# Performance work log

Hardware: AMD Instinct MI355X
Metric: run time of the kernel (lower is better)

The kernel has to match this reference:

```python
import jax, jax.numpy as jnp
import numpy as np

L, D, H, G = 3, 64, 4, 64            # layers, hidden_dim, heads, num_graphs
N, E = 20000, 320000                  # nodes, edges
HD = H * D                            # heads * out_channels = 256
DENSE = 256
EPS = 1e-5


def setup_inputs() -> dict:
    key = jax.random.key(0)
    ks = jax.random.split(key, 32)
    s = 0.05
    f32 = jnp.float32
    inp = {
        "x": jax.random.normal(ks[0], (N, D), f32),
        "edge_attr": jax.random.normal(ks[1], (E, D), f32),
        "edge_index": jax.random.randint(ks[2], (2, E), 0, N, dtype=jnp.int32),
        "batch": ((jnp.arange(N, dtype=jnp.int32) * G) // N).astype(jnp.int32),
        # per-layer TransformerConv params (stacked over layer dim)
        "Wq": jax.random.normal(ks[3], (L, D, HD), f32) * s,
        "bq": jnp.zeros((L, HD), f32),
        "Wk": jax.random.normal(ks[4], (L, D, HD), f32) * s,
        "bk": jnp.zeros((L, HD), f32),
        "Wv": jax.random.normal(ks[5], (L, D, HD), f32) * s,
        "bv": jnp.zeros((L, HD), f32),
        "We": jax.random.normal(ks[6], (L, D, HD), f32) * s,   # lin_edge (no bias in PyG)
        "Wskip": jax.random.normal(ks[7], (L, D, HD), f32) * s,
        "bskip": jnp.zeros((L, HD), f32),
        "bn_gamma": jnp.ones((L, HD), f32),
        "bn_beta": jnp.zeros((L, HD), f32),
        "Wt": jax.random.normal(ks[8], (L, HD, D), f32) * s,   # transf_layers
        "bt": jnp.zeros((L, D), f32),
        # MLP head
        "W1": jax.random.normal(ks[9], (2 * D, DENSE), f32) * s,
        "b1": jnp.zeros((DENSE,), f32),
        "W2": jax.random.normal(ks[10], (DENSE, DENSE // 2), f32) * s,
        "b2": jnp.zeros((DENSE // 2,), f32),
        "W3": jax.random.normal(ks[11], (DENSE // 2, 1), f32) * s,
        "b3": jnp.zeros((1,), f32),
    }
    return inp


def _transformer_conv(x, edge_attr, src, dst, Wq, bq, Wk, bk, Wv, bv, We, Wskip, bskip):
    # PyG TransformerConv, concat=True, beta=False, root_weight=True, eval (no attn dropout)
    q = (x @ Wq + bq).reshape(N, H, D)[dst]                 # [E,H,C]
    k = (x @ Wk + bk).reshape(N, H, D)[src]                 # [E,H,C]
    v = (x @ Wv + bv).reshape(N, H, D)[src]                 # [E,H,C]
    e = (edge_attr @ We).reshape(E, H, D)                   # [E,H,C]
    k = k + e
    logits = (q * k).sum(-1) / jnp.sqrt(jnp.asarray(D, x.dtype))  # [E,H]
    m = jax.ops.segment_max(logits, dst, num_segments=N)    # stable softmax per dst node
    p = jnp.exp(logits - m[dst])
    z = jax.ops.segment_sum(p, dst, num_segments=N)
    w = p / z[dst]                                          # [E,H]
    msg = w[..., None] * (v + e)                            # [E,H,C]
    agg = jax.ops.segment_sum(msg, dst, num_segments=N).reshape(N, HD)
    return agg + x @ Wskip + bskip                          # [N, H*C]


def _batchnorm(h, gamma, beta):
    mu = h.mean(0)
    var = h.var(0)  # biased, as torch BN uses for normalization
    return (h - mu) * jax.lax.rsqrt(var + EPS) * gamma + beta


def reference(x, edge_attr, edge_index, batch, Wq, bq, Wk, bk, Wv, bv, We, Wskip,
              bskip, bn_gamma, bn_beta, Wt, bt, W1, b1, W2, b2, W3, b3):
    src, dst = edge_index[0], edge_index[1]
    counts = jax.ops.segment_sum(jnp.ones((N,), x.dtype), batch, num_segments=G)
    rep = jnp.zeros((G, 2 * D), x.dtype)
    for i in range(L):
        h = _transformer_conv(x, edge_attr, src, dst, Wq[i], bq[i], Wk[i], bk[i],
                              Wv[i], bv[i], We[i], Wskip[i], bskip[i])
        h = _batchnorm(h, bn_gamma[i], bn_beta[i])
        x = jax.nn.relu(h @ Wt[i] + bt[i])                  # [N, D]
        gmx = jax.ops.segment_max(x, batch, num_segments=G)
        gav = jax.ops.segment_sum(x, batch, num_segments=G) / counts[:, None]
        rep = rep + jnp.concatenate([gmx, gav], axis=1)     # sum of per-layer reps
    out = jax.nn.relu(rep @ W1 + b1)
    out = jax.nn.relu(out @ W2 + b2)
    return out @ W3 + b3                                    # [G, 1]
```

## Files before the change

kernel.cpp:

```cpp
#include <hip/hip_runtime.h>
#include <math.h>
#include <float.h>

#define N_NODES 20000
#define N_PAD 20032
#define N_EDGES 320000
#define NGRAPH 64
#define NLAYER 3
#define BN_EPS 1e-5f

typedef short bf16x8 __attribute__((ext_vector_type(8)));
typedef float f32x4 __attribute__((ext_vector_type(4)));
typedef unsigned short u16x8 __attribute__((ext_vector_type(8)));

__device__ inline unsigned short f2bf(float f) {
    unsigned int u = __float_as_uint(f);
    unsigned int r = u + 0x7FFF + ((u >> 16) & 1);
    return (unsigned short)(r >> 16);
}
__device__ inline float bf2f(unsigned short s) {
    return __uint_as_float((unsigned int)s << 16);
}

__global__ void count_kernel(const int* __restrict__ ei, int* __restrict__ cnt) {
    int e = blockIdx.x * blockDim.x + threadIdx.x;
    if (e < N_EDGES) atomicAdd(&cnt[ei[N_EDGES + e]], 1);
}

__global__ void scan_kernel(const int* __restrict__ cnt, int* __restrict__ rowptr) {
    __shared__ int sh[256];
    int t = threadIdx.x;
    const int CH = (N_NODES + 255) / 256;
    int base = t * CH;
    int s = 0;
    for (int i = 0; i < CH; i++) { int idx = base + i; if (idx < N_NODES) s += cnt[idx]; }
    sh[t] = s;
    __syncthreads();
    for (int off = 1; off < 256; off <<= 1) {
        int v = sh[t];
        int add = (t >= off) ? sh[t - off] : 0;
        __syncthreads();
        sh[t] = v + add;
        __syncthreads();
    }
    int run = sh[t] - s;
    for (int i = 0; i < CH; i++) {
        int idx = base + i;
        if (idx < N_NODES) { rowptr[idx] = run; run += cnt[idx]; }
    }
    if (t == 255) rowptr[N_NODES] = sh[255];
}

__global__ void fill_kernel(const int* __restrict__ ei, const int* __restrict__ rowptr,
                            int* __restrict__ cur, int* __restrict__ eidx,
                            int* __restrict__ esrc) {
    int e = blockIdx.x * blockDim.x + threadIdx.x;
    if (e < N_EDGES) {
        int dst = ei[N_EDGES + e];
        int pos = atomicAdd(&cur[dst], 1);
        int slot = rowptr[dst] + pos;
        eidx[slot] = e;
        esrc[slot] = ei[e];
    }
}

__global__ void permute_ea_b_kernel(const float* __restrict__ edge_attr,
                                    const int* __restrict__ eidx,
                                    unsigned short* __restrict__ eaPb) {
    int idx = blockIdx.x * blockDim.x + threadIdx.x;
    if (idx < N_EDGES * 16) {
        int j = idx >> 4, c4 = idx & 15;
        float4 v = *(const float4*)(edge_attr + (size_t)eidx[j] * 64 + c4 * 4);
        ((ushort4*)eaPb)[idx] = make_ushort4(f2bf(v.x), f2bf(v.y), f2bf(v.z), f2bf(v.w));
    }
}

__global__ void wu_kernel(const float* __restrict__ Wq, const float* __restrict__ bq,
                          const float* __restrict__ We,
                          float* __restrict__ Wu, float* __restrict__ bu) {
    int j = blockIdx.x, layer = blockIdx.y;
    int t = threadIdx.x, h = t >> 6, d = t & 63;
    const float* Wql = Wq + layer * 16384;
    const float* Wel = We + layer * 16384;
    float acc = 0.f;
    for (int c = 0; c < 64; c++)
        acc += Wql[j * 256 + h * 64 + c] * Wel[d * 256 + h * 64 + c];
    Wu[layer * 16384 + j * 256 + h * 64 + d] = acc;
    if (j == 0) {
        const float* bql = bq + layer * 256;
        float ab = 0.f;
        for (int c = 0; c < 64; c++) ab += bql[h * 64 + c] * Wel[d * 256 + h * 64 + c];
        bu[layer * 256 + h * 64 + d] = ab;
    }
}

__global__ void wallt_kernel(const float* __restrict__ Wq, const float* __restrict__ Wk,
                             const float* __restrict__ Wv, const float* __restrict__ Ws,
                             const float* __restrict__ Wu,
                             const float* __restrict__ bq, const float* __restrict__ bk,
                             const float* __restrict__ bv, const float* __restrict__ bs,
                             const float* __restrict__ bu,
                             unsigned short* __restrict__ WallT, float* __restrict__ ball) {
    int c = blockIdx.x, l = blockIdx.y, k = threadIdx.x;
    int seg = c >> 8, ci = c & 255;
    const float* W; const float* b;
    switch (seg) {
        case 0:  W = Wq; b = bq; break;
        case 1:  W = Wk; b = bk; break;
        case 2:  W = Wv; b = bv; break;
        case 3:  W = Ws; b = bs; break;
        default: W = Wu; b = bu; break;
    }
    WallT[(size_t)l * 81920 + c * 64 + k] = f2bf(W[l * 16384 + k * 256 + ci]);
    if (k == 0) ball[l * 1280 + c] = b[l * 256 + ci];
}

__global__ void xtobf_kernel(const float* __restrict__ x, unsigned short* __restrict__ xbf) {
    int i4 = blockIdx.x * 256 + threadIdx.x;
    if (i4 >= N_PAD * 64 / 4) return;
    int n = i4 >> 4;
    ushort4 o;
    if (n < N_NODES) {
        float4 v = ((const float4*)x)[i4];
        o = make_ushort4(f2bf(v.x), f2bf(v.y), f2bf(v.z), f2bf(v.w));
    } else o = make_ushort4(0, 0, 0, 0);
    ((ushort4*)xbf)[i4] = o;
}

__global__ __launch_bounds__(256) void gemm_qkvsu2_kernel(
    const unsigned short* __restrict__ xbf,
    const unsigned short* __restrict__ WallT,
    const float* __restrict__ ball,
    unsigned short* __restrict__ qbf, unsigned short* __restrict__ kvbf,
    unsigned short* __restrict__ sbf, unsigned short* __restrict__ ubf) {
    int t = threadIdx.x, wid = t >> 6, lane = t & 63;
    int lrow = lane & 15, lk = lane >> 4;
    int y = blockIdx.y;
    int col0 = y * 64;
    int q = y & 3;
    unsigned short* outp; int ostr, mul, obase;
    if (y < 4)       { outp = qbf;  ostr = 256; mul = 1; obase = q * 64; }
    else if (y < 8)  { outp = kvbf; ostr = 512; mul = 2; obase = q * 128; }
    else if (y < 12) { outp = kvbf; ostr = 512; mul = 2; obase = q * 128 + 1; }
    else if (y < 16) { outp = sbf;  ostr = 256; mul = 1; obase = q * 64; }
    else             { outp = ubf;  ostr = 256; mul = 1; obase = q * 64; }

    bf16x8 bfrag[4][2];
#pragma unroll
    for (int ct = 0; ct < 4; ct++)
#pragma unroll
        for (int kc = 0; kc < 2; kc++)
            bfrag[ct][kc] = *(const bf16x8*)(WallT +
                (size_t)(col0 + ct * 16 + lrow) * 64 + kc * 32 + lk * 8);
    float bias[4];
#pragma unroll
    for (int ct = 0; ct < 4; ct++) bias[ct] = ball[col0 + ct * 16 + lrow];

    for (int nc = blockIdx.x; nc < N_PAD / 64; nc += gridDim.x) {
        int n0 = nc * 64 + wid * 16;
        bf16x8 a0 = *(const bf16x8*)(xbf + (size_t)(n0 + lrow) * 64 + lk * 8);
        bf16x8 a1 = *(const bf16x8*)(xbf + (size_t)(n0 + lrow) * 64 + 32 + lk * 8);
#pragma unroll
        for (int ct = 0; ct < 4; ct++) {
            f32x4 acc = {bias[ct], bias[ct], bias[ct], bias[ct]};
            acc = __builtin_amdgcn_mfma_f32_16x16x32_bf16(a0, bfrag[ct][0], acc, 0, 0, 0);
            acc = __builtin_amdgcn_mfma_f32_16x16x32_bf16(a1, bfrag[ct][1], acc, 0, 0, 0);
            int cl = ct * 16 + lrow;
#pragma unroll
            for (int r = 0; r < 4; r++) {
                int n = n0 + lk * 4 + r;
                if (n < N_NODES)
                    outp[(size_t)n * ostr + obase + cl * mul] = f2bf(acc[r]);
            }
        }
    }
}

__global__ __launch_bounds__(256) void attn6_kernel(
    const unsigned short* __restrict__ eaPb,
    const float* __restrict__ ea_f32,
    const int* __restrict__ eaidx,
    const int* __restrict__ rowptr, const int* __restrict__ esrc,
    const unsigned short* __restrict__ qbf, const unsigned short* __restrict__ ubf,
    const unsigned short* __restrict__ kvbf,
    const unsigned short* __restrict__ sbf,
    unsigned short* __restrict__ hskb,
    unsigned short* __restrict__ raccb) {
    int t = threadIdx.x;
    int wid = t >> 6, lane = t & 63;
    int c4 = lane * 4;
    int ec4 = (lane & 15) * 4;
    for (int n = blockIdx.x * 4 + wid; n < N_NODES; n += gridDim.x * 4) {
        ushort4 qu = *(const ushort4*)(qbf + (size_t)n * 256 + c4);
        ushort4 uu = *(const ushort4*)(ubf + (size_t)n * 256 + c4);
        float4 q4 = make_float4(bf2f(qu.x), bf2f(qu.y), bf2f(qu.z), bf2f(qu.w));
        float4 u4 = make_float4(bf2f(uu.x), bf2f(uu.y), bf2f(uu.z), bf2f(uu.w));
        int j0 = rowptr[n];
        int cnt = rowptr[n + 1] - j0;
        float l = 0.f;
        float4 a4 = make_float4(0.f, 0.f, 0.f, 0.f), r4 = a4;
        u16x8 kvA = {0, 0, 0, 0, 0, 0, 0, 0}, kvB = kvA;
        float4 eA = make_float4(0.f, 0.f, 0.f, 0.f), eB = eA;

#define LOADE(KV, EV, JJ) do { \
        int _j = j0 + (JJ); \
        int _s = __builtin_amdgcn_readfirstlane(esrc[_j]); \
        KV = *(const u16x8*)(kvbf + (size_t)_s * 512 + c4 * 2); \
        if (eaPb) { ushort4 _e = *(const ushort4*)(eaPb + (size_t)_j * 64 + ec4); \
                    EV = make_float4(bf2f(_e.x), bf2f(_e.y), bf2f(_e.z), bf2f(_e.w)); } \
        else { EV = *(const float4*)(ea_f32 + (size_t)eaidx[_j] * 64 + ec4); } \
    } while (0)

#define PROC(KV, EV) do { \
        float p = q4.x * bf2f(KV[0]) + q4.y * bf2f(KV[2]) \
                + q4.z * bf2f(KV[4]) + q4.w * bf2f(KV[6]) \
                + u4.x * EV.x + u4.y * EV.y + u4.z * EV.z + u4.w * EV.w; \
        p += __shfl_xor(p, 1); p += __shfl_xor(p, 2); \
        p += __shfl_xor(p, 4); p += __shfl_xor(p, 8); \
        p = __expf(p * 0.125f); \
        l += p; \
        a4.x += p * bf2f(KV[1]); a4.y += p * bf2f(KV[3]); \
        a4.z += p * bf2f(KV[5]); a4.w += p * bf2f(KV[7]); \
        r4.x += p * EV.x; r4.y += p * EV.y; r4.z += p * EV.z; r4.w += p * EV.w; \
    } while (0)

        if (cnt > 0) LOADE(kvA, eA, 0);
        if (cnt > 1) LOADE(kvB, eB, 1);
        int jj = 0;
        for (; jj + 1 < cnt; jj += 2) {
            u16x8 kv0 = kvA; float4 e0 = eA;
            if (jj + 2 < cnt) LOADE(kvA, eA, jj + 2);
            PROC(kv0, e0);
            u16x8 kv1 = kvB; float4 e1 = eB;
            if (jj + 3 < cnt) LOADE(kvB, eB, jj + 3);
            PROC(kv1, e1);
        }
        if (jj < cnt) PROC(kvA, eA);
#undef LOADE
#undef PROC
        float inv = (l > 0.f) ? 1.f / l : 0.f;
        ushort4 su = *(const ushort4*)(sbf + (size_t)n * 256 + c4);
        *(ushort4*)(hskb + (size_t)n * 256 + c4) = make_ushort4(
            f2bf(a4.x * inv + bf2f(su.x)), f2bf(a4.y * inv + bf2f(su.y)),
            f2bf(a4.z * inv + bf2f(su.z)), f2bf(a4.w * inv + bf2f(su.w)));
        *(ushort4*)(raccb + (size_t)n * 256 + c4) = make_ushort4(
            f2bf(r4.x * inv), f2bf(r4.y * inv), f2bf(r4.z * inv), f2bf(r4.w * inv));
    }
}

__global__ __launch_bounds__(256) void msgbn2_kernel(
    const unsigned short* __restrict__ raccb, const float* __restrict__ We,
    const unsigned short* __restrict__ hskb, unsigned short* __restrict__ hbf,
    float* __restrict__ statsL) {
    int t = threadIdx.x;
    float wcol[64];
#pragma unroll
    for (int d = 0; d < 64; d++) wcol[d] = We[d * 256 + t];
    int hoff = t & 192;
    float s = 0.f, s2 = 0.f;
    for (int n = blockIdx.x * 4; n < N_NODES; n += gridDim.x * 4) {
#pragma unroll
        for (int ni = 0; ni < 4; ni++) {
            const unsigned short* rrow = raccb + (size_t)(n + ni) * 256 + hoff;
            float acc = 0.f;
#pragma unroll
            for (int d4 = 0; d4 < 64; d4 += 4) {
                ushort4 r4 = *(const ushort4*)(rrow + d4);
                acc += bf2f(r4.x) * wcol[d4] + bf2f(r4.y) * wcol[d4 + 1]
                     + bf2f(r4.z) * wcol[d4 + 2] + bf2f(r4.w) * wcol[d4 + 3];
            }
            float hv = bf2f(hskb[(size_t)(n + ni) * 256 + t]) + acc;
            hbf[(size_t)(n + ni) * 256 + t] = f2bf(hv);
            s += hv; s2 += hv * hv;
        }
    }
    int base = (blockIdx.x & 7) * 512;
    atomicAdd(&statsL[base + t], s);
    atomicAdd(&statsL[base + 256 + t], s2);
}

__global__ __launch_bounds__(256) void bn_fold4_kernel(
    const float* __restrict__ statsL,
    const float* __restrict__ gamma, const float* __restrict__ beta,
    const float* __restrict__ Wt, const float* __restrict__ bt,
    unsigned short* __restrict__ WtpT,
    float* __restrict__ biasp) {
    __shared__ float aL[256], bbL[256], part[256];
    int t = threadIdx.x;
    float sum = 0.f, sq = 0.f;
#pragma unroll
    for (int s = 0; s < 8; s++) {
        sum += statsL[s * 512 + t];
        sq  += statsL[s * 512 + 256 + t];
    }
    float mean = sum * (1.f / N_NODES);
    float var = sq * (1.f / N_NODES) - mean * mean;
    float a = rsqrtf(var + BN_EPS) * gamma[t];
    aL[t] = a;
    bbL[t] = beta[t] - mean * a;
    __syncthreads();
    for (int i = t; i < 16384; i += 256) {
        int k = i >> 6, o = i & 63;
        WtpT[o * 256 + k] = f2bf(aL[k] * Wt[i]);
    }
    float p = 0.f;
    int o = t & 63, kq = (t >> 6) * 64;
    for (int kk = kq; kk < kq + 64; kk++) p += bbL[kk] * Wt[kk * 64 + o];
    part[t] = p;
    __syncthreads();
    if (t < 64) biasp[t] = bt[t] + part[t] + part[64 + t] + part[128 + t] + part[192 + t];
}

__global__ __launch_bounds__(256) void xform4_kernel(
    const unsigned short* __restrict__ hbf,
    const unsigned short* __restrict__ WtpT,
    const float* __restrict__ biasp,
    unsigned short* __restrict__ xbf,
    float* __restrict__ poolmx, float* __restrict__ poolsm, int layer) {
    __shared__ float xt[64][65];
    __shared__ float red[4][2][2][64];
    int t = threadIdx.x, wid = t >> 6, lane = t & 63;
    int lrow = lane & 15, lk = lane >> 4;
    bf16x8 bfrag[4][8];
#pragma unroll
    for (int ct = 0; ct < 4; ct++)
#pragma unroll
        for (int kc = 0; kc < 8; kc++)
            bfrag[ct][kc] = *(const bf16x8*)(WtpT +
                (size_t)(ct * 16 + lrow) * 256 + kc * 32 + lk * 8);
    float bias[4];
#pragma unroll
    for (int ct = 0; ct < 4; ct++) bias[ct] = biasp[ct * 16 + lrow];

    for (int nc = blockIdx.x; nc < N_PAD / 64; nc += gridDim.x) {
        int n0 = nc * 64;
        int nw = n0 + wid * 16;
        f32x4 acc[4];
#pragma unroll
        for (int ct = 0; ct < 4; ct++)
            acc[ct] = {bias[ct], bias[ct], bias[ct], bias[ct]};
#pragma unroll
        for (int kc = 0; kc < 8; kc++) {
            bf16x8 a = *(const bf16x8*)(hbf + (size_t)(nw + lrow) * 256 + kc * 32 + lk * 8);
#pragma unroll
            for (int ct = 0; ct < 4; ct++)
                acc[ct] = __builtin_amdgcn_mfma_f32_16x16x32_bf16(a, bfrag[ct][kc], acc[ct], 0, 0, 0);
        }
#pragma unroll
        for (int ct = 0; ct < 4; ct++) {
            int c = ct * 16 + lrow;
#pragma unroll
            for (int r = 0; r < 4; r++) {
                int n = nw + lk * 4 + r;
                float v = fmaxf(acc[ct][r], 0.f);
                xt[wid * 16 + lk * 4 + r][c] = v;
                if (n < N_NODES) xbf[(size_t)n * 64 + c] = f2bf(v);
            }
        }
        __syncthreads();
        int g0 = (n0 * 64) / 20000;
        int b = ((20000 * (g0 + 1) + 63) >> 6) - n0;
        if (b > 64) b = 64;
        {
            int ch = t & 63, rp = t >> 6;
            float mx0 = 0.f, sm0 = 0.f, mx1 = 0.f, sm1 = 0.f;
            for (int r = rp * 16; r < rp * 16 + 16; r++) {
                if (n0 + r < N_NODES) {
                    float v = xt[r][ch];
                    if (r < b) { mx0 = fmaxf(mx0, v); sm0 += v; }
                    else       { mx1 = fmaxf(mx1, v); sm1 += v; }
                }
            }
            red[rp][0][0][ch] = mx0; red[rp][0][1][ch] = sm0;
            red[rp][1][0][ch] = mx1; red[rp][1][1][ch] = sm1;
        }
        __syncthreads();
        if (t < 128) {
            int seg = t >> 6, ch = t & 63;
            float m = red[0][seg][0][ch], s = red[0][seg][1][ch];
#pragma unroll
            for (int w = 1; w < 4; w++) {
                m = fmaxf(m, red[w][seg][0][ch]);
                s += red[w][seg][1][ch];
            }
            int g = g0 + seg;
            bool valid = (seg == 0) || (b < 64 && g < NGRAPH);
            if (valid) {
                atomicMax((unsigned int*)&poolmx[(layer * NGRAPH + g) * 64 + ch],
                          __float_as_uint(m));
                atomicAdd(&poolsm[(layer * NGRAPH + g) * 64 + ch], s);
            }
        }
        __syncthreads();
    }
}

__global__ __launch_bounds__(256) void head_kernel(
    const float* __restrict__ poolmx, const float* __restrict__ poolsm,
    const float* __restrict__ W1, const float* __restrict__ b1,
    const float* __restrict__ W2, const float* __restrict__ b2,
    const float* __restrict__ W3, const float* __restrict__ b3,
    float* __restrict__ out) {
    int g = blockIdx.x, t = threadIdx.x;
    __shared__ float repL[128], o1sh[256], o2sh[128];
    if (t < 128) {
        int d = t & 63;
        int start = (N_NODES * g + 63) >> 6;
        int end = (N_NODES * (g + 1) + 63) >> 6;
        float v = 0.f;
        if (t < 64) {
#pragma unroll
            for (int l = 0; l < NLAYER; l++) v += poolmx[(l * NGRAPH + g) * 64 + d];
        } else {
            float inv = 1.f / (float)(end - start);
#pragma unroll
            for (int l = 0; l < NLAYER; l++) v += poolsm[(l * NGRAPH + g) * 64 + d] * inv;
        }
        repL[t] = v;
    }
    __syncthreads();
    float a1 = b1[t];
    for (int k = 0; k < 128; k++) a1 += repL[k] * W1[k * 256 + t];
    o1sh[t] = fmaxf(a1, 0.f);
    __syncthreads();
    if (t < 128) {
        float a2 = b2[t];
        for (int k = 0; k < 256; k++) a2 += o1sh[k] * W2[k * 128 + t];
        o2sh[t] = fmaxf(a2, 0.f);
    }
    __syncthreads();
    if (t < 64) {
        float p = o2sh[t] * W3[t] + o2sh[t + 64] * W3[t + 64];
#pragma unroll
        for (int off = 32; off; off >>= 1) p += __shfl_xor(p, off);
        if (t == 0) out[g] = p + b3[0];
    }
}

extern "C" void kernel_launch(void* const* d_in, const int* in_sizes, int n_in,
                              void* d_out, int out_size, void* d_ws, size_t ws_size,
                              hipStream_t stream) {
    const float* x         = (const float*)d_in[0];
    const float* edge_attr = (const float*)d_in[1];
    const int*   ei        = (const int*)d_in[2];
    const float* Wq  = (const float*)d_in[4];
    const float* bq  = (const float*)d_in[5];
    const float* Wk  = (const float*)d_in[6];
    const float* bk  = (const float*)d_in[7];
    const float* Wv  = (const float*)d_in[8];
    const float* bv  = (const float*)d_in[9];
    const float* We  = (const float*)d_in[10];
    const float* Wsk = (const float*)d_in[11];
    const float* bsk = (const float*)d_in[12];
    const float* gam = (const float*)d_in[13];
    const float* bet = (const float*)d_in[14];
    const float* Wt  = (const float*)d_in[15];
    const float* bt  = (const float*)d_in[16];
    const float* W1  = (const float*)d_in[17];
    const float* b1  = (const float*)d_in[18];
    const float* W2  = (const float*)d_in[19];
    const float* b2  = (const float*)d_in[20];
    const float* W3  = (const float*)d_in[21];
    const float* b3  = (const float*)d_in[22];
    float* out = (float*)d_out;

    char* ws = (char*)d_ws;
    size_t off = 0;
    auto alloc = [&](size_t bytes) -> char* {
        char* p = ws + off;
        off += (bytes + 255) & ~(size_t)255;
        return p;
    };
    int*   rowptr = (int*)alloc((N_NODES + 1) * sizeof(int));
    int*   eidx   = (int*)alloc((size_t)N_EDGES * sizeof(int));
    int*   esrc   = (int*)alloc((size_t)N_EDGES * sizeof(int));
    unsigned short* qbf  = (unsigned short*)alloc((size_t)N_NODES * 256 * 2);
    unsigned short* kvbf = (unsigned short*)alloc((size_t)N_NODES * 512 * 2);
    unsigned short* sbf  = (unsigned short*)alloc((size_t)N_NODES * 256 * 2);
    unsigned short* ubf  = (unsigned short*)alloc((size_t)N_NODES * 256 * 2);
    unsigned short* hskb = (unsigned short*)alloc((size_t)N_NODES * 256 * 2);
    unsigned short* raccb= (unsigned short*)alloc((size_t)N_NODES * 256 * 2);
    unsigned short* hbf  = (unsigned short*)alloc((size_t)N_PAD * 256 * 2);
    unsigned short* xbf  = (unsigned short*)alloc((size_t)N_PAD * 64 * 2);
    unsigned short* WtpT = (unsigned short*)alloc(64 * 256 * 2);
    float* biasp  = (float*)alloc(64 * sizeof(float));
    float* Wu     = (float*)alloc((size_t)NLAYER * 16384 * sizeof(float));
    float* bu     = (float*)alloc((size_t)NLAYER * 256 * sizeof(float));
    unsigned short* WallT = (unsigned short*)alloc((size_t)NLAYER * 81920 * 2);
    float* ball   = (float*)alloc((size_t)NLAYER * 1280 * sizeof(float));
    size_t zero_off = off;
    int*   cur1   = (int*)alloc(N_NODES * sizeof(int));
    int*   cur2   = (int*)alloc(N_NODES * sizeof(int));
    float* statsA = (float*)alloc((size_t)NLAYER * 8 * 512 * sizeof(float));
    float* poolmx = (float*)alloc((size_t)NLAYER * NGRAPH * 64 * sizeof(float));
    float* poolsm = (float*)alloc((size_t)NLAYER * NGRAPH * 64 * sizeof(float));
    size_t zero_bytes = off - zero_off;
    unsigned short* eaPb = (unsigned short*)alloc((size_t)N_EDGES * 64 * 2);
    bool perm = (off <= ws_size);

    hipMemsetAsync(ws + zero_off, 0, zero_bytes, stream);

    count_kernel<<<(N_EDGES + 255) / 256, 256, 0, stream>>>(ei, cur1);
    scan_kernel<<<1, 256, 0, stream>>>(cur1, rowptr);
    fill_kernel<<<(N_EDGES + 255) / 256, 256, 0, stream>>>(ei, rowptr, cur2, eidx, esrc);
    if (perm) {
        permute_ea_b_kernel<<<(N_EDGES * 16 + 255) / 256, 256, 0, stream>>>(
            edge_attr, eidx, eaPb);
    }

    wu_kernel<<<dim3(64, NLAYER), 256, 0, stream>>>(Wq, bq, We, Wu, bu);
    wallt_kernel<<<dim3(1280, NLAYER), 64, 0, stream>>>(
        Wq, Wk, Wv, Wsk, Wu, bq, bk, bv, bsk, bu, WallT, ball);
    xtobf_kernel<<<(N_PAD * 64 / 4 + 255) / 256, 256, 0, stream>>>(x, xbf);

    for (int i = 0; i < NLAYER; i++) {
        gemm_qkvsu2_kernel<<<dim3(79, 20), 256, 0, stream>>>(
            xbf, WallT + (size_t)i * 81920, ball + i * 1280, qbf, kvbf, sbf, ubf);

        attn6_kernel<<<2500, 256, 0, stream>>>(
            perm ? eaPb : (const unsigned short*)nullptr, edge_attr,
            eidx, rowptr, esrc, qbf, ubf, kvbf, sbf, hskb, raccb);

        msgbn2_kernel<<<1250, 256, 0, stream>>>(
            raccb, We + i * 16384, hskb, hbf, statsA + (size_t)i * 4096);

        bn_fold4_kernel<<<1, 256, 0, stream>>>(
            statsA + (size_t)i * 4096, gam + i * 256, bet + i * 256,
            Wt + i * 16384, bt + i * 64, WtpT, biasp);

        xform4_kernel<<<157, 256, 0, stream>>>(
            hbf, WtpT, biasp, xbf, poolmx, poolsm, i);
    }

    head_kernel<<<64, 256, 0, stream>>>(poolmx, poolsm, W1, b1, W2, b2, W3, b3, out);
}
```

Before: 685.6 us.

## Deepen attention edge prefetch to four, widen GEMM column groups, parallelize BN fold

The attention kernel now keeps four edges' key/value and edge-attribute loads in flight instead of two, and holds edge attributes as bf16 until use, aiming to hide gather latency better. The QKV GEMM kernel handles two 64-column groups per block, halving grid.y so each A-fragment load is reused across eight MFMA tiles. The BN fold kernel is split across eight blocks for the weight rescale, with block 0 alone computing the bias. The costs are more registers in the attention and GEMM kernels, which may lower occupancy, and a small padding of the edge-source buffer.

Result: slower. 715.2 us (+4.3%).

```diff
diff --git a/kernel.cpp b/kernel.cpp
--- a/kernel.cpp
+++ b/kernel.cpp
@@ -127,7 +127,7 @@
     ((ushort4*)xbf)[i4] = o;
 }
 
-__global__ __launch_bounds__(256) void gemm_qkvsu2_kernel(
+__global__ __launch_bounds__(256) void gemm_qkvsu3_kernel(
     const unsigned short* __restrict__ xbf,
     const unsigned short* __restrict__ WallT,
     const float* __restrict__ ball,
@@ -135,48 +135,54 @@
     unsigned short* __restrict__ sbf, unsigned short* __restrict__ ubf) {
     int t = threadIdx.x, wid = t >> 6, lane = t & 63;
     int lrow = lane & 15, lk = lane >> 4;
-    int y = blockIdx.y;
-    int col0 = y * 64;
-    int q = y & 3;
-    unsigned short* outp; int ostr, mul, obase;
-    if (y < 4)       { outp = qbf;  ostr = 256; mul = 1; obase = q * 64; }
-    else if (y < 8)  { outp = kvbf; ostr = 512; mul = 2; obase = q * 128; }
-    else if (y < 12) { outp = kvbf; ostr = 512; mul = 2; obase = q * 128 + 1; }
-    else if (y < 16) { outp = sbf;  ostr = 256; mul = 1; obase = q * 64; }
-    else             { outp = ubf;  ostr = 256; mul = 1; obase = q * 64; }
-
-    bf16x8 bfrag[4][2];
-#pragma unroll
-    for (int ct = 0; ct < 4; ct++)
-#pragma unroll
-        for (int kc = 0; kc < 2; kc++)
-            bfrag[ct][kc] = *(const bf16x8*)(WallT +
-                (size_t)(col0 + ct * 16 + lrow) * 64 + kc * 32 + lk * 8);
-    float bias[4];
-#pragma unroll
-    for (int ct = 0; ct < 4; ct++) bias[ct] = ball[col0 + ct * 16 + lrow];
+
+    bf16x8 bfrag[2][4][2];
+    float bias[2][4];
+    unsigned short* outp[2]; int ostr[2], mul[2], obase[2];
+#pragma unroll
+    for (int cg = 0; cg < 2; cg++) {
+        int ys = blockIdx.y * 2 + cg;
+        int col0 = ys * 64;
+        int q = ys & 3;
+        if (ys < 4)       { outp[cg] = qbf;  ostr[cg] = 256; mul[cg] = 1; obase[cg] = q * 64; }
+        else if (ys < 8)  { outp[cg] = kvbf; ostr[cg] = 512; mul[cg] = 2; obase[cg] = q * 128; }
+        else if (ys < 12) { outp[cg] = kvbf; ostr[cg] = 512; mul[cg] = 2; obase[cg] = q * 128 + 1; }
+        else if (ys < 16) { outp[cg] = sbf;  ostr[cg] = 256; mul[cg] = 1; obase[cg] = q * 64; }
+        else              { outp[cg] = ubf;  ostr[cg] = 256; mul[cg] = 1; obase[cg] = q * 64; }
+#pragma unroll
+        for (int ct = 0; ct < 4; ct++) {
+#pragma unroll
+            for (int kc = 0; kc < 2; kc++)
+                bfrag[cg][ct][kc] = *(const bf16x8*)(WallT +
+                    (size_t)(col0 + ct * 16 + lrow) * 64 + kc * 32 + lk * 8);
+            bias[cg][ct] = ball[col0 + ct * 16 + lrow];
+        }
+    }
 
     for (int nc = blockIdx.x; nc < N_PAD / 64; nc += gridDim.x) {
         int n0 = nc * 64 + wid * 16;
         bf16x8 a0 = *(const bf16x8*)(xbf + (size_t)(n0 + lrow) * 64 + lk * 8);
         bf16x8 a1 = *(const bf16x8*)(xbf + (size_t)(n0 + lrow) * 64 + 32 + lk * 8);
 #pragma unroll
-        for (int ct = 0; ct < 4; ct++) {
-            f32x4 acc = {bias[ct], bias[ct], bias[ct], bias[ct]};
-            acc = __builtin_amdgcn_mfma_f32_16x16x32_bf16(a0, bfrag[ct][0], acc, 0, 0, 0);
-            acc = __builtin_amdgcn_mfma_f32_16x16x32_bf16(a1, bfrag[ct][1], acc, 0, 0, 0);
-            int cl = ct * 16 + lrow;
-#pragma unroll
-            for (int r = 0; r < 4; r++) {
-                int n = n0 + lk * 4 + r;
-                if (n < N_NODES)
-                    outp[(size_t)n * ostr + obase + cl * mul] = f2bf(acc[r]);
+        for (int cg = 0; cg < 2; cg++) {
+#pragma unroll
+            for (int ct = 0; ct < 4; ct++) {
+                f32x4 acc = {bias[cg][ct], bias[cg][ct], bias[cg][ct], bias[cg][ct]};
+                acc = __builtin_amdgcn_mfma_f32_16x16x32_bf16(a0, bfrag[cg][ct][0], acc, 0, 0, 0);
+                acc = __builtin_amdgcn_mfma_f32_16x16x32_bf16(a1, bfrag[cg][ct][1], acc, 0, 0, 0);
+                int cl = ct * 16 + lrow;
+#pragma unroll
+                for (int r = 0; r < 4; r++) {
+                    int n = n0 + lk * 4 + r;
+                    if (n < N_NODES)
+                        outp[cg][(size_t)n * ostr[cg] + obase[cg] + cl * mul[cg]] = f2bf(acc[r]);
+                }
             }
         }
     }
 }
 
-__global__ __launch_bounds__(256) void attn6_kernel(
+__global__ __launch_bounds__(256) void attn7_kernel(
     const unsigned short* __restrict__ eaPb,
     const float* __restrict__ ea_f32,
     const int* __restrict__ eaidx,
@@ -199,43 +205,46 @@
         int cnt = rowptr[n + 1] - j0;
         float l = 0.f;
         float4 a4 = make_float4(0.f, 0.f, 0.f, 0.f), r4 = a4;
-        u16x8 kvA = {0, 0, 0, 0, 0, 0, 0, 0}, kvB = kvA;
-        float4 eA = make_float4(0.f, 0.f, 0.f, 0.f), eB = eA;
+        u16x8 kv0 = {0,0,0,0,0,0,0,0}, kv1 = kv0, kv2 = kv0, kv3 = kv0;
+        ushort4 e0 = make_ushort4(0,0,0,0), e1 = e0, e2 = e0, e3 = e0;
 
 #define LOADE(KV, EV, JJ) do { \
         int _j = j0 + (JJ); \
         int _s = __builtin_amdgcn_readfirstlane(esrc[_j]); \
         KV = *(const u16x8*)(kvbf + (size_t)_s * 512 + c4 * 2); \
-        if (eaPb) { ushort4 _e = *(const ushort4*)(eaPb + (size_t)_j * 64 + ec4); \
-                    EV = make_float4(bf2f(_e.x), bf2f(_e.y), bf2f(_e.z), bf2f(_e.w)); } \
-        else { EV = *(const float4*)(ea_f32 + (size_t)eaidx[_j] * 64 + ec4); } \
+        if (eaPb) { EV = *(const ushort4*)(eaPb + (size_t)_j * 64 + ec4); } \
+        else { float4 _f = *(const float4*)(ea_f32 + (size_t)eaidx[_j] * 64 + ec4); \
+               EV = make_ushort4(f2bf(_f.x), f2bf(_f.y), f2bf(_f.z), f2bf(_f.w)); } \
     } while (0)
 
 #define PROC(KV, EV) do { \
+        float ex = bf2f(EV.x), ey = bf2f(EV.y), ez = bf2f(EV.z), ew = bf2f(EV.w); \
         float p = q4.x * bf2f(KV[0]) + q4.y * bf2f(KV[2]) \
                 + q4.z * bf2f(KV[4]) + q4.w * bf2f(KV[6]) \
-                + u4.x * EV.x + u4.y * EV.y + u4.z * EV.z + u4.w * EV.w; \
+                + u4.x * ex + u4.y * ey + u4.z * ez + u4.w * ew; \
         p += __shfl_xor(p, 1); p += __shfl_xor(p, 2); \
         p += __shfl_xor(p, 4); p += __shfl_xor(p, 8); \
         p = __expf(p * 0.125f); \
         l += p; \
         a4.x += p * bf2f(KV[1]); a4.y += p * bf2f(KV[3]); \
         a4.z += p * bf2f(KV[5]); a4.w += p * bf2f(KV[7]); \
-        r4.x += p * EV.x; r4.y += p * EV.y; r4.z += p * EV.z; r4.w += p * EV.w; \
+        r4.x += p * ex; r4.y += p * ey; r4.z += p * ez; r4.w += p * ew; \
     } while (0)
 
-        if (cnt > 0) LOADE(kvA, eA, 0);
-        if (cnt > 1) LOADE(kvB, eB, 1);
+        if (cnt > 0) LOADE(kv0, e0, 0);
+        if (cnt > 1) LOADE(kv1, e1, 1);
+        if (cnt > 2) LOADE(kv2, e2, 2);
+        if (cnt > 3) LOADE(kv3, e3, 3);
         int jj = 0;
-        for (; jj + 1 < cnt; jj += 2) {
-            u16x8 kv0 = kvA; float4 e0 = eA;
-            if (jj + 2 < cnt) LOADE(kvA, eA, jj + 2);
-            PROC(kv0, e0);
-            u16x8 kv1 = kvB; float4 e1 = eB;
-            if (jj + 3 < cnt) LOADE(kvB, eB, jj + 3);
-            PROC(kv1, e1);
-        }
-        if (jj < cnt) PROC(kvA, eA);
+        for (; jj + 3 < cnt; jj += 4) {
+            PROC(kv0, e0); if (jj + 4 < cnt) LOADE(kv0, e0, jj + 4);
+            PROC(kv1, e1); if (jj + 5 < cnt) LOADE(kv1, e1, jj + 5);
+            PROC(kv2, e2); if (jj + 6 < cnt) LOADE(kv2, e2, jj + 6);
+            PROC(kv3, e3); if (jj + 7 < cnt) LOADE(kv3, e3, jj + 7);
+        }
+        if (jj < cnt)     PROC(kv0, e0);
+        if (jj + 1 < cnt) PROC(kv1, e1);
+        if (jj + 2 < cnt) PROC(kv2, e2);
 #undef LOADE
 #undef PROC
         float inv = (l > 0.f) ? 1.f / l : 0.f;
@@ -279,7 +288,7 @@
     atomicAdd(&statsL[base + 256 + t], s2);
 }
 
-__global__ __launch_bounds__(256) void bn_fold4_kernel(
+__global__ __launch_bounds__(256) void bn_fold5_kernel(
     const float* __restrict__ statsL,
     const float* __restrict__ gamma, const float* __restrict__ beta,
     const float* __restrict__ Wt, const float* __restrict__ bt,
@@ -299,16 +308,19 @@
     aL[t] = a;
     bbL[t] = beta[t] - mean * a;
     __syncthreads();
-    for (int i = t; i < 16384; i += 256) {
+    int i0 = blockIdx.x * 2048;
+    for (int i = i0 + t; i < i0 + 2048; i += 256) {
         int k = i >> 6, o = i & 63;
         WtpT[o * 256 + k] = f2bf(aL[k] * Wt[i]);
     }
-    float p = 0.f;
-    int o = t & 63, kq = (t >> 6) * 64;
-    for (int kk = kq; kk < kq + 64; kk++) p += bbL[kk] * Wt[kk * 64 + o];
-    part[t] = p;
-    __syncthreads();
-    if (t < 64) biasp[t] = bt[t] + part[t] + part[64 + t] + part[128 + t] + part[192 + t];
+    if (blockIdx.x == 0) {
+        float p = 0.f;
+        int o = t & 63, kq = (t >> 6) * 64;
+        for (int kk = kq; kk < kq + 64; kk++) p += bbL[kk] * Wt[kk * 64 + o];
+        part[t] = p;
+        __syncthreads();
+        if (t < 64) biasp[t] = bt[t] + part[t] + part[64 + t] + part[128 + t] + part[192 + t];
+    }
 }
 
 __global__ __launch_bounds__(256) void xform4_kernel(
@@ -473,7 +485,7 @@
     };
     int*   rowptr = (int*)alloc((N_NODES + 1) * sizeof(int));
     int*   eidx   = (int*)alloc((size_t)N_EDGES * sizeof(int));
-    int*   esrc   = (int*)alloc((size_t)N_EDGES * sizeof(int));
+    int*   esrc   = (int*)alloc(((size_t)N_EDGES + 16) * sizeof(int));
     unsigned short* qbf  = (unsigned short*)alloc((size_t)N_NODES * 256 * 2);
     unsigned short* kvbf = (unsigned short*)alloc((size_t)N_NODES * 512 * 2);
     unsigned short* sbf  = (unsigned short*)alloc((size_t)N_NODES * 256 * 2);
@@ -514,17 +526,17 @@
     xtobf_kernel<<<(N_PAD * 64 / 4 + 255) / 256, 256, 0, stream>>>(x, xbf);
 
     for (int i = 0; i < NLAYER; i++) {
-        gemm_qkvsu2_kernel<<<dim3(79, 20), 256, 0, stream>>>(
+        gemm_qkvsu3_kernel<<<dim3(79, 10), 256, 0, stream>>>(
             xbf, WallT + (size_t)i * 81920, ball + i * 1280, qbf, kvbf, sbf, ubf);
 
-        attn6_kernel<<<2500, 256, 0, stream>>>(
+        attn7_kernel<<<2500, 256, 0, stream>>>(
             perm ? eaPb : (const unsigned short*)nullptr, edge_attr,
             eidx, rowptr, esrc, qbf, ubf, kvbf, sbf, hskb, raccb);
 
         msgbn2_kernel<<<1250, 256, 0, stream>>>(
             raccb, We + i * 16384, hskb, hbf, statsA + (size_t)i * 4096);
 
-        bn_fold4_kernel<<<1, 256, 0, stream>>>(
+        bn_fold5_kernel<<<8, 256, 0, stream>>>(
             statsA + (size_t)i * 4096, gam + i * 256, bet + i * 256,
             Wt + i * 16384, bt + i * 64, WtpT, biasp);
 
```
